# Kernel optimization log

Hardware: AMD Instinct MI355X
Metric: run time of the kernel (lower is better)

Reference implementation:

```python
import jax, jax.numpy as jnp
import numpy as np

ALPHA = 0.2          # LeakyReLU negative slope
NEG_FILL = -9e15     # mask value used by the original module


def setup_inputs() -> dict:
    key = jax.random.key(0)
    k1, k2, k3, k4 = jax.random.split(key, 4)
    N, D, H, F = 4096, 512, 8, 64  # nhid*nheads == embedding_dim
    h = jax.random.normal(k1, (N, D), dtype=jnp.float32)
    adj = jax.random.randint(k2, (N, N), 0, 2, dtype=jnp.int32)
    # per-head linear projection weights (no bias) and attention vectors
    W = jax.random.normal(k3, (H, D, F), dtype=jnp.float32) * (1.0 / np.sqrt(D))
    a = jax.random.normal(k4, (H, 2 * F), dtype=jnp.float32) * 0.1
    return {"h": h, "adj": adj, "W": W, "a": a}


def reference(h, adj, W, a):
    H, D, F = W.shape
    N = h.shape[0]
    # per-head projection: [H, N, F]
    hp = jnp.einsum('nd,hdf->hnf', h, W)
    # score(i,j) = leakyrelu(a[:F].h_i + a[F:].h_j)  (decomposed broadcast-add,
    # same math as the original N*N concat construction)
    a_src, a_dst = a[:, :F], a[:, F:]
    f_src = jnp.einsum('hnf,hf->hn', hp, a_src)  # [H, N]
    f_dst = jnp.einsum('hnf,hf->hn', hp, a_dst)  # [H, N]
    e = jax.nn.leaky_relu(f_src[:, :, None] + f_dst[:, None, :], ALPHA)  # [H,N,N]
    e = jnp.where(adj[None] > 0, e, NEG_FILL)
    att = jax.nn.softmax(e, axis=-1)  # softmax over neighbors j (dim=1 in torch)
    out = jnp.einsum('hij,hjf->hif', att, hp)  # [H, N, F]
    # concat heads -> [N, H*F], then ELU
    out = jnp.transpose(out, (1, 0, 2)).reshape(N, H * F)
    return jax.nn.elu(out)
```

## Files before the change

### kernel.cpp

```cpp
#include <hip/hip_runtime.h>

#define NN 4096
#define DD 512
#define HH 8
#define FF 64
#define LRELU_ALPHA 0.2f
#define SP 72

typedef __attribute__((ext_vector_type(8))) short bf16x8;
typedef __attribute__((ext_vector_type(4))) float f32x4;

__device__ __forceinline__ float f4c(const float4& v, int k) {
    return k == 0 ? v.x : (k == 1 ? v.y : (k == 2 ? v.z : v.w));
}
__device__ __forceinline__ void f4s(float4& v, int k, float x) {
    if (k == 0) v.x = x; else if (k == 1) v.y = x; else if (k == 2) v.z = x; else v.w = x;
}
__device__ __forceinline__ unsigned short f2bf(float x) {
    unsigned u = __float_as_uint(x);
    return (unsigned short)((u + 0x7fffu + ((u >> 16) & 1u)) >> 16);
}
__device__ __forceinline__ float bf2f(unsigned short h) {
    return __uint_as_float(((unsigned)h) << 16);
}
__device__ __forceinline__ unsigned fkey(float x) {
    unsigned u = __float_as_uint(x);
    return (u & 0x80000000u) ? ~u : (u | 0x80000000u);
}
__device__ __forceinline__ float funkey(unsigned k) {
    unsigned u = (k & 0x80000000u) ? (k ^ 0x80000000u) : ~k;
    return __uint_as_float(u);
}
__device__ __forceinline__ void sync_lds() {
    asm volatile("s_waitcnt lgkmcnt(0)\n\ts_barrier" ::: "memory");
}

__global__ __launch_bounds__(256) void k_prep(const int* __restrict__ adj,
                                              const float* __restrict__ W,
                                              unsigned* __restrict__ adjw,
                                              unsigned short* __restrict__ wt_hi,
                                              unsigned short* __restrict__ wt_lo,
                                              unsigned* __restrict__ mxkey,
                                              float* __restrict__ hpsum) {
    __shared__ float tile[64][65];
    int b = blockIdx.x, t = threadIdx.x;
    if (b < 4096) {
        int lane = t & 63;
        #pragma unroll
        for (int i = 0; i < 16; i++) {
            int tid = ((b * 16 + i) << 8) + t;
            unsigned long long mask = __ballot(adj[tid] > 0);
            if (lane == 0) {
                int base = tid >> 5;
                adjw[base] = (unsigned)mask;
                adjw[base + 1] = (unsigned)(mask >> 32);
            }
        }
    } else if (b < 4160) {
        int idx = b - 4096;
        int h = idx >> 3;
        int d0 = (idx & 7) * 64;
        #pragma unroll
        for (int kidx = 0; kidx < 4; kidx++) {
            int id = t + 256 * kidx;
            int dd = id >> 4, f4i = (id & 15) * 4;
            float4 v = *(const float4*)(W + ((size_t)(h * DD + d0 + dd)) * FF + f4i);
            tile[dd][f4i] = v.x; tile[dd][f4i + 1] = v.y;
            tile[dd][f4i + 2] = v.z; tile[dd][f4i + 3] = v.w;
        }
        __syncthreads();
        int f = t >> 2, c = (t & 3) * 16;
        union { unsigned short s[16]; uint4 v[2]; } hb, lb;
        #pragma unroll
        for (int q = 0; q < 16; q++) {
            float v = tile[c + q][f];
            unsigned short hi = f2bf(v);
            hb.s[q] = hi;
            lb.s[q] = f2bf(v - bf2f(hi));
        }
        uint4* dh = (uint4*)(wt_hi + ((size_t)h * FF + f) * DD + d0 + c);
        uint4* dl = (uint4*)(wt_lo + ((size_t)h * FF + f) * DD + d0 + c);
        dh[0] = hb.v[0]; dh[1] = hb.v[1];
        dl[0] = lb.v[0]; dl[1] = lb.v[1];
    } else {
        if (t < 16) mxkey[t] = 0u;
        hpsum[t] = 0.f;
        hpsum[t + 256] = 0.f;
    }
}

__global__ __launch_bounds__(256) void k_hp_mfma(const float* __restrict__ hmat,
                                                 const unsigned short* __restrict__ whi,
                                                 const unsigned short* __restrict__ wlo,
                                                 const float* __restrict__ a,
                                                 unsigned short* __restrict__ hpT_hi,
                                                 float* __restrict__ fs,
                                                 float* __restrict__ fd,
                                                 float* __restrict__ hpsum,
                                                 unsigned* __restrict__ mxkey) {
    __shared__ char smem[4 * 64 * SP * 2];
    unsigned short* ah = (unsigned short*)smem;
    unsigned short* al = ah + 64 * SP;
    unsigned short* bh = al + 64 * SP;
    unsigned short* bl = bh + 64 * SP;

    int t = threadIdx.x;
    int h = blockIdx.y;
    int n0 = blockIdx.x * 64;
    int lane = t & 63;
    int w = t >> 6;
    int R0 = (w >> 1) * 32, F0 = (w & 1) * 32;
    int am = lane & 15, aq = lane >> 4;
    int sr = t >> 2, sc = (t & 3) * 16;

    const float* gha = hmat + (size_t)(n0 + sr) * DD;
    const unsigned short* gbh = whi + ((size_t)h * FF + sr) * DD;
    const unsigned short* gbl = wlo + ((size_t)h * FF + sr) * DD;

    float4 p0, p1, p2, p3;
    uint4 w0, w1, x0, x1;
    auto gload = [&](int kk) {
        p0 = *(const float4*)(gha + kk + sc);
        p1 = *(const float4*)(gha + kk + sc + 4);
        p2 = *(const float4*)(gha + kk + sc + 8);
        p3 = *(const float4*)(gha + kk + sc + 12);
        const uint4* s2 = (const uint4*)(gbh + kk + sc);
        const uint4* s3 = (const uint4*)(gbl + kk + sc);
        w0 = s2[0]; w1 = s2[1]; x0 = s3[0]; x1 = s3[1];
    };
    auto wstage = [&]() {
        union { unsigned short s[16]; uint4 v[2]; } hb, lb;
        #pragma unroll
        for (int q = 0; q < 16; q++) {
            float v = q < 4 ? f4c(p0, q) : q < 8 ? f4c(p1, q - 4)
                      : q < 12 ? f4c(p2, q - 8) : f4c(p3, q - 12);
            unsigned short hi = f2bf(v);
            hb.s[q] = hi;
            lb.s[q] = f2bf(v - bf2f(hi));
        }
        *(uint4*)(ah + sr * SP + sc) = hb.v[0]; *(uint4*)(ah + sr * SP + sc + 8) = hb.v[1];
        *(uint4*)(al + sr * SP + sc) = lb.v[0]; *(uint4*)(al + sr * SP + sc + 8) = lb.v[1];
        *(uint4*)(bh + sr * SP + sc) = w0; *(uint4*)(bh + sr * SP + sc + 8) = w1;
        *(uint4*)(bl + sr * SP + sc) = x0; *(uint4*)(bl + sr * SP + sc + 8) = x1;
    };

    f32x4 acc[2][2] = {};
    gload(0);
    for (int kk = 0; kk < DD; kk += 64) {
        wstage();
        if (kk + 64 < DD) gload(kk + 64);
        sync_lds();
        #pragma unroll
        for (int k2 = 0; k2 < 2; k2++) {
            int ko = k2 * 32 + aq * 8;
            bf16x8 a0h = *(const bf16x8*)(ah + (R0 + am) * SP + ko);
            bf16x8 a1h = *(const bf16x8*)(ah + (R0 + 16 + am) * SP + ko);
            bf16x8 a0l = *(const bf16x8*)(al + (R0 + am) * SP + ko);
            bf16x8 a1l = *(const bf16x8*)(al + (R0 + 16 + am) * SP + ko);
            bf16x8 b0h = *(const bf16x8*)(bh + (F0 + am) * SP + ko);
            bf16x8 b1h = *(const bf16x8*)(bh + (F0 + 16 + am) * SP + ko);
            bf16x8 b0l = *(const bf16x8*)(bl + (F0 + am) * SP + ko);
            bf16x8 b1l = *(const bf16x8*)(bl + (F0 + 16 + am) * SP + ko);
            acc[0][0] = __builtin_amdgcn_mfma_f32_16x16x32_bf16(a0h, b0h, acc[0][0], 0, 0, 0);
            acc[0][1] = __builtin_amdgcn_mfma_f32_16x16x32_bf16(a0h, b1h, acc[0][1], 0, 0, 0);
            acc[1][0] = __builtin_amdgcn_mfma_f32_16x16x32_bf16(a1h, b0h, acc[1][0], 0, 0, 0);
            acc[1][1] = __builtin_amdgcn_mfma_f32_16x16x32_bf16(a1h, b1h, acc[1][1], 0, 0, 0);
            acc[0][0] = __builtin_amdgcn_mfma_f32_16x16x32_bf16(a0h, b0l, acc[0][0], 0, 0, 0);
            acc[0][1] = __builtin_amdgcn_mfma_f32_16x16x32_bf16(a0h, b1l, acc[0][1], 0, 0, 0);
            acc[1][0] = __builtin_amdgcn_mfma_f32_16x16x32_bf16(a1h, b0l, acc[1][0], 0, 0, 0);
            acc[1][1] = __builtin_amdgcn_mfma_f32_16x16x32_bf16(a1h, b1l, acc[1][1], 0, 0, 0);
            acc[0][0] = __builtin_amdgcn_mfma_f32_16x16x32_bf16(a0l, b0h, acc[0][0], 0, 0, 0);
            acc[0][1] = __builtin_amdgcn_mfma_f32_16x16x32_bf16(a0l, b1h, acc[0][1], 0, 0, 0);
            acc[1][0] = __builtin_amdgcn_mfma_f32_16x16x32_bf16(a1l, b0h, acc[1][0], 0, 0, 0);
            acc[1][1] = __builtin_amdgcn_mfma_f32_16x16x32_bf16(a1l, b1h, acc[1][1], 0, 0, 0);
        }
        sync_lds();
    }

    unsigned* tt = (unsigned*)smem;
    float* rs = (float*)(smem + 17408);
    float* rd = rs + 256;
    float* ash = rd + 256;
    if (t < 128) ash[t] = a[h * 2 * FF + t];
    int col = lane & 15, rbase = (lane >> 4) * 4;
    #pragma unroll
    for (int m16 = 0; m16 < 2; m16++) {
        #pragma unroll
        for (int n16 = 0; n16 < 2; n16++) {
            #pragma unroll
            for (int r = 0; r < 4; r++) {
                int nl = R0 + m16 * 16 + rbase + r;
                int f = F0 + n16 * 16 + col;
                float v = acc[m16][n16][r];
                unsigned short hi = f2bf(v);
                unsigned short lo = f2bf(v - bf2f(hi));
                tt[f * 68 + nl] = (unsigned)hi | ((unsigned)lo << 16);
            }
        }
    }
    __syncthreads();
    {
        int f = t >> 2, c = (t & 3) * 16;
        union { unsigned short s[16]; uint4 v[2]; } hb;
        float csum = 0.f;
        #pragma unroll
        for (int q = 0; q < 16; q++) {
            unsigned u = tt[f * 68 + c + q];
            hb.s[q] = (unsigned short)(u & 0xffffu);
            csum += bf2f((unsigned short)(u & 0xffffu)) + bf2f((unsigned short)(u >> 16));
        }
        uint4* dh = (uint4*)(hpT_hi + ((size_t)h * FF + f) * NN + n0 + c);
        dh[0] = hb.v[0]; dh[1] = hb.v[1];
        csum += __shfl_xor(csum, 1);
        csum += __shfl_xor(csum, 2);
        if ((t & 3) == 0) unsafeAtomicAdd(hpsum + h * FF + f, csum);
    }
    {
        int n = t & 63, g = t >> 6;
        float fsp = 0.f, fdp = 0.f;
        #pragma unroll
        for (int q = 0; q < 16; q++) {
            int f = g * 16 + q;
            unsigned u = tt[f * 68 + n];
            float v = bf2f((unsigned short)(u & 0xffffu)) + bf2f((unsigned short)(u >> 16));
            fsp += v * ash[f];
            fdp += v * ash[64 + f];
        }
        rs[g * 64 + n] = fsp;
        rd[g * 64 + n] = fdp;
    }
    __syncthreads();
    if (t < 64) {
        float fdv = rd[t] + rd[64 + t] + rd[128 + t] + rd[192 + t];
        fs[(size_t)h * NN + n0 + t] = rs[t] + rs[64 + t] + rs[128 + t] + rs[192 + t];
        fd[(size_t)h * NN + n0 + t] = fdv;
        unsigned key = fkey(fdv);
        #pragma unroll
        for (int off = 32; off; off >>= 1) key = max(key, (unsigned)__shfl_xor((int)key, off));
        if (t == 0) atomicMax(mxkey + h, key);
    }
}

__global__ __launch_bounds__(256) void k_attn(const float* __restrict__ fs,
                                              const float* __restrict__ fd,
                                              const unsigned* __restrict__ mxkey,
                                              const unsigned* __restrict__ adjw,
                                              const unsigned short* __restrict__ hpT_hi,
                                              const float* __restrict__ hpsum,
                                              float* __restrict__ outp) {
    __shared__ unsigned short hbh[2][64 * SP];

    int t = threadIdx.x;
    int h = blockIdx.y;
    int wv = t >> 6;
    int q0 = blockIdx.x * 64 + wv * 16;
    int lane = t & 63;
    int am = lane & 15, aq = lane >> 4;
    int sr = t >> 2, sc = (t & 3) * 16;

    const float LOG2E = 1.44269504f;
    float mfd = funkey(mxkey[h]);
    float fsr = fs[(size_t)h * NN + q0 + am];
    float sM = fsr + mfd;
    float mr = fmaxf(sM, LRELU_ALPHA * sM) * LOG2E;
    float Ac = __builtin_fmaf(fsr, LOG2E, -mr);
    float Bc = __builtin_fmaf(fsr, LRELU_ALPHA * LOG2E, -mr);

    const unsigned short* gH = hpT_hi + ((size_t)h * FF + sr) * NN + sc;
    const float* pfd = fd + (size_t)h * NN + aq * 8;
    const unsigned* prow = adjw + (size_t)(q0 + am) * (NN / 32);
    int bsh = aq * 8;

    f32x4 acc[4] = {};
    f32x4 accl = {};
    bf16x8 bones;
    #pragma unroll
    for (int i = 0; i < 8; i++) bones[i] = (short)0x3f80;

    uint4 H0, H1;
    float4 XFa0, XFa1, XFb0, XFb1; uint2 XAw;
    float4 YFa0, YFa1, YFb0, YFb1; uint2 YAw;

    auto gloadH = [&](int j0) {
        H0 = *(const uint4*)(gH + j0);
        H1 = *(const uint4*)(gH + j0 + 8);
    };
    auto gloadFX = [&](int j0) {
        XFa0 = *(const float4*)(pfd + j0);
        XFa1 = *(const float4*)(pfd + j0 + 4);
        XFb0 = *(const float4*)(pfd + j0 + 32);
        XFb1 = *(const float4*)(pfd + j0 + 36);
        XAw  = *(const uint2*)(prow + (j0 >> 5));
    };
    auto gloadFY = [&](int j0) {
        YFa0 = *(const float4*)(pfd + j0);
        YFa1 = *(const float4*)(pfd + j0 + 4);
        YFb0 = *(const float4*)(pfd + j0 + 32);
        YFb1 = *(const float4*)(pfd + j0 + 36);
        YAw  = *(const uint2*)(prow + (j0 >> 5));
    };
    auto wstageH = [&](int buf) {
        *(uint4*)(&hbh[buf][sr * SP + sc]) = H0;
        *(uint4*)(&hbh[buf][sr * SP + sc + 8]) = H1;
    };
    auto agen = [&](float4 f0, float4 f1, unsigned word) -> bf16x8 {
        unsigned bits = word >> bsh;
        unsigned eu[8];
        #pragma unroll
        for (int q = 0; q < 2; q++) {
            float4 fdv = q ? f1 : f0;
            #pragma unroll
            for (int b = 0; b < 4; b++) {
                float fdL = f4c(fdv, b) * LOG2E;
                float t1 = Ac + fdL;
                float t2 = __builtin_fmaf(fdL, LRELU_ALPHA, Bc);
                float e = __builtin_amdgcn_exp2f(fmaxf(t1, t2));
                e = ((bits >> (q * 4 + b)) & 1u) ? e : 0.f;
                eu[q * 4 + b] = __float_as_uint(e);
            }
        }
        union { unsigned u[4]; bf16x8 v; } af;
        af.u[0] = __builtin_amdgcn_perm(eu[1], eu[0], 0x07060302);
        af.u[1] = __builtin_amdgcn_perm(eu[3], eu[2], 0x07060302);
        af.u[2] = __builtin_amdgcn_perm(eu[5], eu[4], 0x07060302);
        af.u[3] = __builtin_amdgcn_perm(eu[7], eu[6], 0x07060302);
        return af.v;
    };
    auto mfma_tile = [&](int buf, bf16x8 afA, bf16x8 afB) {
        {
            int ko = aq * 8;
            bf16x8 b0 = *(const bf16x8*)(&hbh[buf][(am) * SP + ko]);
            bf16x8 b1 = *(const bf16x8*)(&hbh[buf][(16 + am) * SP + ko]);
            bf16x8 b2 = *(const bf16x8*)(&hbh[buf][(32 + am) * SP + ko]);
            bf16x8 b3 = *(const bf16x8*)(&hbh[buf][(48 + am) * SP + ko]);
            acc[0] = __builtin_amdgcn_mfma_f32_16x16x32_bf16(afA, b0, acc[0], 0, 0, 0);
            acc[1] = __builtin_amdgcn_mfma_f32_16x16x32_bf16(afA, b1, acc[1], 0, 0, 0);
            acc[2] = __builtin_amdgcn_mfma_f32_16x16x32_bf16(afA, b2, acc[2], 0, 0, 0);
            acc[3] = __builtin_amdgcn_mfma_f32_16x16x32_bf16(afA, b3, acc[3], 0, 0, 0);
            accl   = __builtin_amdgcn_mfma_f32_16x16x32_bf16(afA, bones, accl, 0, 0, 0);
        }
        {
            int ko = 32 + aq * 8;
            bf16x8 b0 = *(const bf16x8*)(&hbh[buf][(am) * SP + ko]);
            bf16x8 b1 = *(const bf16x8*)(&hbh[buf][(16 + am) * SP + ko]);
            bf16x8 b2 = *(const bf16x8*)(&hbh[buf][(32 + am) * SP + ko]);
            bf16x8 b3 = *(const bf16x8*)(&hbh[buf][(48 + am) * SP + ko]);
            acc[0] = __builtin_amdgcn_mfma_f32_16x16x32_bf16(afB, b0, acc[0], 0, 0, 0);
            acc[1] = __builtin_amdgcn_mfma_f32_16x16x32_bf16(afB, b1, acc[1], 0, 0, 0);
            acc[2] = __builtin_amdgcn_mfma_f32_16x16x32_bf16(afB, b2, acc[2], 0, 0, 0);
            acc[3] = __builtin_amdgcn_mfma_f32_16x16x32_bf16(afB, b3, acc[3], 0, 0, 0);
            accl   = __builtin_amdgcn_mfma_f32_16x16x32_bf16(afB, bones, accl, 0, 0, 0);
        }
    };

    const int NIT = NN / 64;
    gloadH(0); gloadFX(0);
    wstageH(0);
    gloadH(64); gloadFY(64);
    sync_lds();
    for (int kk = 0; kk < NIT; kk += 2) {
        {
            bf16x8 afA = agen(XFa0, XFa1, XAw.x);
            bf16x8 afB = agen(XFb0, XFb1, XAw.y);
            mfma_tile(0, afA, afB);
            wstageH(1);
            if (kk + 2 < NIT) { gloadH((kk + 2) * 64); gloadFX((kk + 2) * 64); }
            sync_lds();
        }
        {
            bf16x8 afA = agen(YFa0, YFa1, YAw.x);
            bf16x8 afB = agen(YFb0, YFb1, YAw.y);
            mfma_tile(1, afA, afB);
            if (kk + 2 < NIT) {
                wstageH(0);
                if (kk + 3 < NIT) { gloadH((kk + 3) * 64); gloadFY((kk + 3) * 64); }
            }
            sync_lds();
        }
    }

    const float invN = 1.0f / NN;
    int col = lane & 15, rbase = (lane >> 4) * 4;
    #pragma unroll
    for (int r = 0; r < 4; r++) {
        int row = q0 + rbase + r;
        float l = accl[r];
        float rl = 1.f / l;
        #pragma unroll
        for (int Fi = 0; Fi < 4; Fi++) {
            int f = Fi * 16 + col;
            float v;
            if (l > 0.f) v = acc[Fi][r] * rl;
            else         v = hpsum[h * FF + f] * invN;
            v = v > 0.f ? v : __expf(v) - 1.f;
            outp[(size_t)row * (HH * FF) + h * FF + f] = v;
        }
    }
}

extern "C" void kernel_launch(void* const* d_in, const int* in_sizes, int n_in,
                              void* d_out, int out_size, void* d_ws, size_t ws_size,
                              hipStream_t stream) {
    const float* hmat = (const float*)d_in[0];
    const int*   adj  = (const int*)d_in[1];
    const float* W    = (const float*)d_in[2];
    const float* a    = (const float*)d_in[3];
    float* out = (float*)d_out;

    char* ws = (char*)d_ws;
    unsigned short* hpT_hi = (unsigned short*)(ws);
    unsigned*       adjw   = (unsigned*)(ws + (4u << 20));
    unsigned short* wt_hi  = (unsigned short*)(ws + (6u << 20));
    unsigned short* wt_lo  = (unsigned short*)(ws + (6u << 20) + (512u << 10));
    float* fs    = (float*)(ws + (7u << 20));
    float* fd    = (float*)(ws + (7u << 20) + (128u << 10));
    unsigned* mxkey = (unsigned*)(ws + (7u << 20) + (256u << 10));
    float* hpsum = (float*)(mxkey + 16);

    k_prep   <<<dim3(4161),          256, 0, stream>>>(adj, W, adjw, wt_hi, wt_lo,
                                                       mxkey, hpsum);
    k_hp_mfma<<<dim3(64, 8),         256, 0, stream>>>(hmat, wt_hi, wt_lo, a,
                                                       hpT_hi, fs, fd, hpsum, mxkey);
    k_attn   <<<dim3(NN / 64, HH),   256, 0, stream>>>(fs, fd, mxkey, adjw,
                                                       hpT_hi, hpsum, out);
}
```

Before: 190.4 us.

## Split attention key dimension across two blocks and combine partials in new kernel

The attention kernel grid gains a z dimension of 2, and each block handles half of the neighbor (j) range. Partial numerators go to a workspace buffer and to the output buffer, and row sums go to a separate buffer. A new combine kernel adds the partials, normalizes, applies the empty-row fallback and ELU, and writes the output. This doubles the block count (512 to 1024) to fill more compute units. The cost is an extra launch and extra global traffic for the partial accumulators. The shared max offset makes the two halves directly addable.

```diff
diff --git a/kernel.cpp b/kernel.cpp
--- a/kernel.cpp
+++ b/kernel.cpp
@@ -246,17 +246,20 @@
                                               const unsigned* __restrict__ mxkey,
                                               const unsigned* __restrict__ adjw,
                                               const unsigned short* __restrict__ hpT_hi,
-                                              const float* __restrict__ hpsum,
-                                              float* __restrict__ outp) {
+                                              float* __restrict__ acc0,
+                                              float* __restrict__ acc1,
+                                              float* __restrict__ lsumbuf) {
     __shared__ unsigned short hbh[2][64 * SP];
 
     int t = threadIdx.x;
     int h = blockIdx.y;
+    int z = blockIdx.z;
     int wv = t >> 6;
     int q0 = blockIdx.x * 64 + wv * 16;
     int lane = t & 63;
     int am = lane & 15, aq = lane >> 4;
     int sr = t >> 2, sc = (t & 3) * 16;
+    int jb = z * (NN / 2);
 
     const float LOG2E = 1.44269504f;
     float mfd = funkey(mxkey[h]);
@@ -266,9 +269,9 @@
     float Ac = __builtin_fmaf(fsr, LOG2E, -mr);
     float Bc = __builtin_fmaf(fsr, LRELU_ALPHA * LOG2E, -mr);
 
-    const unsigned short* gH = hpT_hi + ((size_t)h * FF + sr) * NN + sc;
-    const float* pfd = fd + (size_t)h * NN + aq * 8;
-    const unsigned* prow = adjw + (size_t)(q0 + am) * (NN / 32);
+    const unsigned short* gH = hpT_hi + ((size_t)h * FF + sr) * NN + sc + jb;
+    const float* pfd = fd + (size_t)h * NN + aq * 8 + jb;
+    const unsigned* prow = adjw + (size_t)(q0 + am) * (NN / 32) + (jb >> 5);
     int bsh = aq * 8;
 
     f32x4 acc[4] = {};
@@ -353,7 +356,7 @@
         }
     };
 
-    const int NIT = NN / 64;
+    const int NIT = NN / 2 / 64;
     gloadH(0); gloadFX(0);
     wstageH(0);
     gloadH(64); gloadFY(64);
@@ -379,23 +382,48 @@
         }
     }
 
-    const float invN = 1.0f / NN;
-    int col = lane & 15, rbase = (lane >> 4) * 4;
+    int rbase = (lane >> 4) * 4;
+    if (am == 0) {
+        #pragma unroll
+        for (int r = 0; r < 4; r++)
+            lsumbuf[((size_t)z * HH + h) * NN + q0 + rbase + r] = accl[r];
+    }
+
+    float* accb = z == 0 ? acc0 : acc1;
+    int col = lane & 15;
     #pragma unroll
     for (int r = 0; r < 4; r++) {
         int row = q0 + rbase + r;
-        float l = accl[r];
-        float rl = 1.f / l;
         #pragma unroll
         for (int Fi = 0; Fi < 4; Fi++) {
             int f = Fi * 16 + col;
-            float v;
-            if (l > 0.f) v = acc[Fi][r] * rl;
-            else         v = hpsum[h * FF + f] * invN;
-            v = v > 0.f ? v : __expf(v) - 1.f;
-            outp[(size_t)row * (HH * FF) + h * FF + f] = v;
-        }
-    }
+            accb[((size_t)row * HH + h) * FF + f] = acc[Fi][r];
+        }
+    }
+}
+
+__global__ __launch_bounds__(256) void k_combine(const float* __restrict__ acc0,
+                                                 const float* acc1,
+                                                 const float* __restrict__ lsumbuf,
+                                                 const float* __restrict__ hpsum,
+                                                 float* outp) {
+    int gid = blockIdx.x * 256 + threadIdx.x;
+    int n = gid >> 7;
+    int rem = gid & 127;
+    int h = rem >> 4, f4 = (rem & 15) * 4;
+    float4 v0 = ((const float4*)acc0)[gid];
+    float4 v1 = ((const float4*)acc1)[gid];
+    float l = lsumbuf[(size_t)h * NN + n] + lsumbuf[((size_t)HH + h) * NN + n];
+    float4 o;
+    const float invN = 1.0f / NN;
+    #pragma unroll
+    for (int c = 0; c < 4; c++) {
+        float v;
+        if (l > 0.f) v = (f4c(v0, c) + f4c(v1, c)) / l;
+        else         v = hpsum[h * FF + f4 + c] * invN;
+        f4s(o, c, v > 0.f ? v : __expf(v) - 1.f);
+    }
+    ((float4*)outp)[gid] = o;
 }
 
 extern "C" void kernel_launch(void* const* d_in, const int* in_sizes, int n_in,
@@ -416,11 +444,16 @@
     float* fd    = (float*)(ws + (7u << 20) + (128u << 10));
     unsigned* mxkey = (unsigned*)(ws + (7u << 20) + (256u << 10));
     float* hpsum = (float*)(mxkey + 16);
-
-    k_prep   <<<dim3(4161),          256, 0, stream>>>(adj, W, adjw, wt_hi, wt_lo,
-                                                       mxkey, hpsum);
-    k_hp_mfma<<<dim3(64, 8),         256, 0, stream>>>(hmat, wt_hi, wt_lo, a,
-                                                       hpT_hi, fs, fd, hpsum, mxkey);
-    k_attn   <<<dim3(NN / 64, HH),   256, 0, stream>>>(fs, fd, mxkey, adjw,
-                                                       hpT_hi, hpsum, out);
-}
+    float* lsumbuf = hpsum + 512;
+    float* accb0 = (float*)(ws + (8u << 20));
+    float* accb1 = out;
+
+    k_prep   <<<dim3(4161),            256, 0, stream>>>(adj, W, adjw, wt_hi, wt_lo,
+                                                         mxkey, hpsum);
+    k_hp_mfma<<<dim3(64, 8),           256, 0, stream>>>(hmat, wt_hi, wt_lo, a,
+                                                         hpT_hi, fs, fd, hpsum, mxkey);
+    k_attn   <<<dim3(NN / 64, HH, 2),  256, 0, stream>>>(fs, fd, mxkey, adjw,
+                                                         hpT_hi, accb0, accb1, lsumbuf);
+    k_combine<<<dim3(HH * NN * FF / 4 / 256), 256, 0, stream>>>(accb0, accb1, lsumbuf,
+                                                                hpsum, out);
+}
```

After: 194.6 us. 2.2% more time.
